# Kernel optimization log

Measured on AMD Instinct MI355X. Metric: run time of the kernel, lower is better.

Reference implementation:

```python
import jax, jax.numpy as jnp
import numpy as np

B, N, D = 32, 181, 512          # batch, num_projs (seq len), embed_dim
H, HD = 8, 64                   # heads, head_dim
DEPTH, FFN = 6, 2048            # layers, mlp_ratio*embed_dim
MAXLEN = 181                    # RPE max_len (EncoderLayer default)
LN_EPS = 1e-5


def setup_inputs() -> dict:
    key = jax.random.key(0)
    ks = jax.random.split(key, 16)
    rn = lambda k, s, sc=0.02: (jax.random.normal(k, s, jnp.float32) * sc)
    return {
        "x_0": jax.random.normal(ks[0], (B, N, D), jnp.float32),
        "max_shift": 50,
        "pos_embed": rn(ks[1], (1, N, D)),
        "qkv_w": rn(ks[2], (DEPTH, D, 3 * D)), "qkv_b": jnp.zeros((DEPTH, 3 * D), jnp.float32),
        "out_w": rn(ks[3], (DEPTH, D, D)), "out_b": jnp.zeros((DEPTH, D), jnp.float32),
        "rel_pos": jax.random.normal(ks[4], (DEPTH, 2 * MAXLEN - 1, HD), jnp.float32),
        "rpe_w": rn(ks[5], (DEPTH, HD, 1)),
        "ln1_g": jnp.ones((DEPTH, D), jnp.float32), "ln1_b": jnp.zeros((DEPTH, D), jnp.float32),
        "ffn_w1": rn(ks[6], (DEPTH, D, FFN)), "ffn_b1": jnp.zeros((DEPTH, FFN), jnp.float32),
        "ffn_w2": rn(ks[7], (DEPTH, FFN, D)), "ffn_b2": jnp.zeros((DEPTH, D), jnp.float32),
        "ln2_g": jnp.ones((DEPTH, D), jnp.float32), "ln2_b": jnp.zeros((DEPTH, D), jnp.float32),
        "mlp_w1": rn(ks[8], (D, 64)), "mlp_b1": jnp.zeros((64,), jnp.float32),
        "mlp_w2": rn(ks[9], (64, 1)), "mlp_b2": jnp.zeros((1,), jnp.float32),
    }


def _layer_norm(x, g, b):
    m = jnp.mean(x, -1, keepdims=True)
    v = jnp.mean((x - m) ** 2, -1, keepdims=True)
    return (x - m) * jax.lax.rsqrt(v + LN_EPS) * g + b


def reference(x_0, max_shift, pos_embed, qkv_w, qkv_b, out_w, out_b, rel_pos, rpe_w,
              ln1_g, ln1_b, ffn_w1, ffn_b1, ffn_w2, ffn_b2, ln2_g, ln2_b,
              mlp_w1, mlp_b1, mlp_w2, mlp_b2):
    Bb, T, L = x_0.shape
    n_head = H
    hd = L // n_head
    scale = hd ** -0.5
    max_len = (rel_pos.shape[1] + 1) // 2
    # relative position index table [T, T]
    idx = jnp.arange(T)[None, :] - jnp.arange(T)[:, None] + (max_len - 1)

    x = x_0 + pos_embed
    depth = qkv_w.shape[0]
    for i in range(depth):
        # --- MHA with relative position bias ---
        qkv = (x @ qkv_w[i] + qkv_b[i]).reshape(Bb, T, 3, n_head, hd)
        q, k, v = qkv[:, :, 0], qkv[:, :, 1], qkv[:, :, 2]   # [B,T,H,hd]
        scores = jnp.einsum('bqhd,bkhd->bhqk', q, k) * scale
        bias = (rel_pos[i][idx] @ rpe_w[i])[..., 0]          # [T,T]
        scores = scores + bias[None, None]
        w = jax.nn.softmax(scores, axis=-1)
        attn = jnp.einsum('bhqk,bkhd->bqhd', w, v).reshape(Bb, T, L)
        attn = attn @ out_w[i] + out_b[i]
        x = _layer_norm(x + attn, ln1_g[i], ln1_b[i])
        # --- FFN ---
        h = jax.nn.gelu(x @ ffn_w1[i] + ffn_b1[i], approximate=False)
        h = h @ ffn_w2[i] + ffn_b2[i]
        x = _layer_norm(x + h, ln2_g[i], ln2_b[i])

    # per-projection shift head
    shift = jax.nn.relu(x @ mlp_w1 + mlp_b1) @ mlp_w2 + mlp_b2   # [B,T,1]

    # --- SpatialTransformer: bilinear warp along L only (flow[:,0] == 0) ---
    grid_y = 2.0 * (jnp.arange(T, dtype=jnp.float32) / (T - 1) - 0.5)   # [T]
    grid_x = 2.0 * (jnp.arange(L, dtype=jnp.float32) / (L - 1) - 0.5)   # [L]
    flow_x = shift * max_shift / (L // 2)                               # [B,T,1]
    gx = grid_x[None, None, :] + flow_x                                 # [B,T,L]
    # unnormalize (align_corners=False), border padding -> clamp coords
    ix = jnp.clip(((gx + 1.0) * L - 1.0) / 2.0, 0.0, L - 1.0)
    iy = jnp.clip(((grid_y + 1.0) * T - 1.0) / 2.0, 0.0, T - 1.0)       # [T]
    ix0f = jnp.floor(ix); wx = ix - ix0f
    iy0f = jnp.floor(iy); wy = iy - iy0f
    ix0 = jnp.clip(ix0f.astype(jnp.int32), 0, L - 1)
    ix1 = jnp.clip(ix0 + 1, 0, L - 1)
    iy0 = jnp.clip(iy0f.astype(jnp.int32), 0, T - 1)
    iy1 = jnp.clip(iy0 + 1, 0, T - 1)
    bidx = jnp.arange(Bb)[:, None, None]
    iy0b, iy1b = iy0[None, :, None], iy1[None, :, None]
    v00 = x_0[bidx, iy0b, ix0]; v01 = x_0[bidx, iy0b, ix1]
    v10 = x_0[bidx, iy1b, ix0]; v11 = x_0[bidx, iy1b, ix1]
    wyb = wy[None, :, None]
    warped = (1 - wyb) * ((1 - wx) * v00 + wx * v01) + wyb * ((1 - wx) * v10 + wx * v11)
    return shift, warped
```

## Files before the change

### kernel.cpp

```cpp
#include <hip/hip_runtime.h>
#include <hip/hip_bf16.h>
#include <math.h>

#define M_ROWS 5792
#define NTOK 181
#define NLAYER 6

typedef __attribute__((ext_vector_type(8))) _Float16 f16x8;
typedef __attribute__((ext_vector_type(4))) float f32x4;
typedef __attribute__((ext_vector_type(16))) float f32x16;

__device__ __forceinline__ ushort f2h(float f) {
    union { _Float16 h; ushort u; } v;
    v.h = (_Float16)f;
    return v.u;
}
__device__ __forceinline__ float h2f(ushort u) {
    union { ushort u; _Float16 h; } v; v.u = u;
    return (float)v.h;
}
__device__ __forceinline__ float gelu_f(float v) {
    return 0.5f * v * (1.0f + erff(v * 0.70710678118654752f));
}
__device__ __forceinline__ void async16(const void* g, void* l) {
    __builtin_amdgcn_global_load_lds((const __attribute__((address_space(1))) void*)g,
                                     (__attribute__((address_space(3))) void*)l, 16, 0, 0);
}

__global__ __launch_bounds__(256) void wt_kernel(const float* __restrict__ W,
                                                 ushort* __restrict__ Wt, int K, int N) {
    __shared__ float t[64][65];
    const size_t ls = (size_t)blockIdx.z * K * N;
    const float* Wl = W + ls;
    ushort* Wtl = Wt + ls;
    const int k0 = blockIdx.x * 64, n0 = blockIdx.y * 64;
    const int tr = threadIdx.x >> 6, tc = threadIdx.x & 63;
    #pragma unroll
    for (int i = 0; i < 16; ++i) {
        const int r = i * 4 + tr;
        t[r][tc] = Wl[(size_t)(k0 + r) * N + n0 + tc];
    }
    __syncthreads();
    #pragma unroll
    for (int i = 0; i < 16; ++i) {
        const int r = i * 4 + tr;
        Wtl[(size_t)(n0 + r) * K + k0 + tc] = f2h(t[tc][r]);
    }
}

__global__ void add_pos_kernel(const float* __restrict__ x0, const float* __restrict__ pos,
                               float* __restrict__ x, ushort* __restrict__ xb) {
    int idx = blockIdx.x * 256 + threadIdx.x;
    const int total = M_ROWS * 128;
    if (idx >= total) return;
    int col = idx & 127;
    int m   = idx >> 7;
    int t   = m % NTOK;
    float4 a = ((const float4*)x0)[idx];
    float4 p = ((const float4*)pos)[t * 128 + col];
    a.x += p.x; a.y += p.y; a.z += p.z; a.w += p.w;
    ((float4*)x)[idx] = a;
    ((ushort4*)xb)[idx] = make_ushort4(f2h(a.x), f2h(a.y), f2h(a.z), f2h(a.w));
}

template<int BM, int EPI, int SK>
__global__ __launch_bounds__(256) void mfma_gemm(const ushort* __restrict__ A,
                                                 const ushort* __restrict__ Bt,
                                                 const float* __restrict__ bias,
                                                 void* __restrict__ Cv,
                                                 int M, int K, int N) {
    constexpr int MREP = BM / 32;
    __shared__ __align__(16) ushort sA[2][BM * 32];
    __shared__ __align__(16) ushort sB[2][128 * 32];

    const int NC  = N >> 7;
    const int NR  = (M + BM - 1) / BM;
    const int NRP = (NR + 7) & ~7;
    const int PSB = NRP * NC;
    const int gid = blockIdx.x;
    const int sk  = (SK > 1) ? gid / PSB : 0;
    const int j   = (SK > 1) ? gid % PSB : gid;
    const int r   = (j / (8 * NC)) * 8 + (j & 7);
    const int c   = (j % (8 * NC)) >> 3;
    if (r >= NR) return;

    const int tid = threadIdx.x;
    const int lane = tid & 63;
    const int w = tid >> 6;
    const int wr = w >> 1, wc = w & 1;
    const int row0 = r * BM, col0 = c * 128;
    const int wbase = tid & ~63;

    f32x4 acc[MREP][4];
    const f32x4 zero = {0.f, 0.f, 0.f, 0.f};
    #pragma unroll
    for (int m = 0; m < MREP; ++m)
        #pragma unroll
        for (int n = 0; n < 4; ++n) acc[m][n] = zero;

    auto stage = [&](int buf, int kt) {
        const int k0 = kt << 5;
        #pragma unroll
        for (int i = 0; i < BM / 64; ++i) {
            const int s = i * 256 + tid;
            const int row = s >> 2;
            const int kbl = (s & 3) ^ ((row >> 1) & 3);
            int gr = row0 + row; if (gr > M - 1) gr = M - 1;
            async16(A + (size_t)gr * K + k0 + (kbl << 3),
                    &sA[buf][(i * 256 + wbase) * 8]);
        }
        #pragma unroll
        for (int i = 0; i < 2; ++i) {
            const int s = i * 256 + tid;
            const int nr = s >> 2;
            const int kbl = (s & 3) ^ ((nr >> 1) & 3);
            async16(Bt + (size_t)(col0 + nr) * K + k0 + (kbl << 3),
                    &sB[buf][(i * 256 + wbase) * 8]);
        }
    };

    const int NIT = (K / SK) >> 5;
    const int kt0 = sk * NIT;
    stage(0, kt0);
    const int l15 = lane & 15, kb = lane >> 4;
    for (int it = 0; it < NIT; ++it) {
        __syncthreads();
        if (it + 1 < NIT) stage((it + 1) & 1, kt0 + it + 1);
        const int buf = it & 1;
        f16x8 af[MREP], bfr[4];
        #pragma unroll
        for (int m = 0; m < MREP; ++m) {
            const int rr = wr * (BM / 2) + m * 16 + l15;
            af[m] = *(const f16x8*)&sA[buf][rr * 32 + ((kb ^ ((rr >> 1) & 3)) << 3)];
        }
        #pragma unroll
        for (int n = 0; n < 4; ++n) {
            const int rr = wc * 64 + n * 16 + l15;
            bfr[n] = *(const f16x8*)&sB[buf][rr * 32 + ((kb ^ ((rr >> 1) & 3)) << 3)];
        }
        #pragma unroll
        for (int m = 0; m < MREP; ++m)
            #pragma unroll
            for (int n = 0; n < 4; ++n)
                acc[m][n] = __builtin_amdgcn_mfma_f32_16x16x32_f16(af[m], bfr[n], acc[m][n], 0, 0, 0);
    }

    const int crow = row0 + wr * (BM / 2) + (lane >> 4) * 4;
    const int ccol = col0 + wc * 64 + l15;
    ushort* outh = (ushort*)Cv + (size_t)sk * M * N;
    #pragma unroll
    for (int m = 0; m < MREP; ++m)
        #pragma unroll
        for (int n = 0; n < 4; ++n) {
            const int gc = ccol + n * 16;
            const float bv = (SK == 1 || sk == 0) ? bias[gc] : 0.f;
            #pragma unroll
            for (int rr = 0; rr < 4; ++rr) {
                const int gr = crow + m * 16 + rr;
                if (gr < M) {
                    float v = acc[m][n][rr] + bv;
                    if (EPI == 1)      outh[(size_t)gr * N + gc] = f2h(gelu_f(v));
                    else if (EPI == 2) outh[(size_t)gr * N + gc] = f2h(v);
                    else               ((float*)Cv)[(size_t)gr * N + gc] = v;
                }
            }
        }
}

__global__ __launch_bounds__(256) void head_mfma(const ushort* __restrict__ A,
                                                 const ushort* __restrict__ Bt,
                                                 const float* __restrict__ b1,
                                                 const float* __restrict__ w2,
                                                 const float* __restrict__ b2,
                                                 float* __restrict__ shift) {
    const int M = M_ROWS, K = 512;
    __shared__ __align__(16) ushort sA[2][128 * 32];
    __shared__ __align__(16) ushort sB[2][64 * 32];
    const int tid = threadIdx.x;
    const int lane = tid & 63;
    const int w = tid >> 6;
    const int row0 = blockIdx.x * 128;
    const int wbase = tid & ~63;

    f32x4 acc[2][4];
    const f32x4 zero = {0.f, 0.f, 0.f, 0.f};
    #pragma unroll
    for (int m = 0; m < 2; ++m)
        #pragma unroll
        for (int n = 0; n < 4; ++n) acc[m][n] = zero;

    auto stage = [&](int buf, int kt) {
        const int k0 = kt << 5;
        #pragma unroll
        for (int i = 0; i < 2; ++i) {
            const int s = i * 256 + tid;
            const int row = s >> 2;
            const int kbl = (s & 3) ^ ((row >> 1) & 3);
            int gr = row0 + row; if (gr > M - 1) gr = M - 1;
            async16(A + (size_t)gr * K + k0 + (kbl << 3),
                    &sA[buf][(i * 256 + wbase) * 8]);
        }
        {
            const int s = tid;
            const int nr = s >> 2;
            const int kbl = (s & 3) ^ ((nr >> 1) & 3);
            async16(Bt + (size_t)nr * K + k0 + (kbl << 3),
                    &sB[buf][wbase * 8]);
        }
    };

    stage(0, 0);
    const int l15 = lane & 15, kb = lane >> 4;
    for (int it = 0; it < 16; ++it) {
        __syncthreads();
        if (it + 1 < 16) stage((it + 1) & 1, it + 1);
        const int buf = it & 1;
        f16x8 af[2], bfr[4];
        #pragma unroll
        for (int m = 0; m < 2; ++m) {
            const int r = w * 32 + m * 16 + l15;
            af[m] = *(const f16x8*)&sA[buf][r * 32 + ((kb ^ ((r >> 1) & 3)) << 3)];
        }
        #pragma unroll
        for (int n = 0; n < 4; ++n) {
            const int r = n * 16 + l15;
            bfr[n] = *(const f16x8*)&sB[buf][r * 32 + ((kb ^ ((r >> 1) & 3)) << 3)];
        }
        #pragma unroll
        for (int m = 0; m < 2; ++m)
            #pragma unroll
            for (int n = 0; n < 4; ++n)
                acc[m][n] = __builtin_amdgcn_mfma_f32_16x16x32_f16(af[m], bfr[n], acc[m][n], 0, 0, 0);
    }

    const float b2v = b2[0];
    float b1v[4], w2v[4];
    #pragma unroll
    for (int n = 0; n < 4; ++n) {
        const int c = n * 16 + l15;
        b1v[n] = b1[c];
        w2v[n] = w2[c];
    }
    #pragma unroll
    for (int m = 0; m < 2; ++m) {
        #pragma unroll
        for (int r = 0; r < 4; ++r) {
            float p = 0.f;
            #pragma unroll
            for (int n = 0; n < 4; ++n)
                p += fmaxf(acc[m][n][r] + b1v[n], 0.f) * w2v[n];
            #pragma unroll
            for (int off = 1; off < 16; off <<= 1) p += __shfl_xor(p, off);
            const int gr = row0 + w * 32 + m * 16 + kb * 4 + r;
            if (l15 == 0 && gr < M) shift[gr] = p + b2v;
        }
    }
}

__global__ void rbias_kernel(const float* __restrict__ rel_pos, const float* __restrict__ rpe_w,
                             float* __restrict__ r) {
    const int l = blockIdx.y;
    int j = blockIdx.x * 64 + threadIdx.x;
    if (j >= 2 * NTOK - 1) return;
    const float* rp = rel_pos + ((size_t)l * (2 * NTOK - 1) + j) * 64;
    const float* wv = rpe_w + l * 64;
    float s = 0.f;
    #pragma unroll
    for (int d = 0; d < 64; d += 4) {
        float4 a = *(const float4*)(rp + d);
        float4 b = *(const float4*)(wv + d);
        s += a.x*b.x + a.y*b.y + a.z*b.z + a.w*b.w;
    }
    r[l * 512 + j] = s;
}

__global__ __launch_bounds__(192, 2) void attn_mfma(const ushort* __restrict__ qkv,
                                                    const float* __restrict__ rb,
                                                    ushort* __restrict__ outb) {
    __shared__ __align__(16) ushort sm[18432];
    __shared__ __align__(16) ushort vt[12288];
    __shared__ float rs[416];
    const int b  = blockIdx.x >> 4;
    const int h  = (blockIdx.x >> 1) & 7;
    const int qh = blockIdx.x & 1;
    const int tid = threadIdx.x, lane = tid & 63, w = tid >> 6;
    const int l31 = lane & 31, hi = lane >> 5;
    const ushort* base = qkv + (size_t)(b * NTOK) * 1536 + h * 64;

    for (int i = tid; i < 416; i += 192) {
        int j = i - 32;
        rs[i] = (j >= 0 && j < 2 * NTOK - 1) ? rb[j] : 0.f;
    }
    #pragma unroll
    for (int i = 0; i < 8; ++i) {
        const int c = i * 192 + w * 64 + lane;
        const int k = c >> 3;
        int kg = k; if (kg > NTOK - 1) kg = NTOK - 1;
        const int dc = (c & 7) ^ (k & 7);
        async16(base + (size_t)kg * 1536 + 512 + dc * 8, &sm[(i * 192 + w * 64) * 8]);
    }
    #pragma unroll
    for (int i = 0; i < 4; ++i) {
        const int c = i * 192 + w * 64 + lane;
        const int ql = c >> 3;
        int qg = qh * 96 + ql; if (qg > NTOK - 1) qg = NTOK - 1;
        const int dc = (c & 7) ^ (ql & 7);
        async16(base + (size_t)qg * 1536 + dc * 8, &sm[12288 + (i * 192 + w * 64) * 8]);
    }
    {
        const int k8 = tid % 24;
        const int dc = tid / 24;
        uint4 rowv[8];
        #pragma unroll
        for (int i = 0; i < 8; ++i) {
            int kk = k8 * 8 + i; if (kk > NTOK - 1) kk = NTOK - 1;
            rowv[i] = *(const uint4*)(base + (size_t)kk * 1536 + 1024 + dc * 8);
        }
        #pragma unroll
        for (int j = 0; j < 8; ++j) {
            const int d = dc * 8 + j;
            const int sd = (d ^ (d >> 3)) & 7;
            uint out[4];
            #pragma unroll
            for (int m = 0; m < 4; ++m) {
                const uint lo  = ((const uint*)&rowv[2 * m    ])[j >> 1];
                const uint hi2 = ((const uint*)&rowv[2 * m + 1])[j >> 1];
                const uint a = (j & 1) ? (lo  >> 16) : (lo  & 0xffffu);
                const uint bb = (j & 1) ? (hi2 >> 16) : (hi2 & 0xffffu);
                out[m] = a | (bb << 16);
            }
            *(uint4*)&vt[d * 192 + ((k8 ^ sd) << 3)] = *(uint4*)out;
        }
    }
    __syncthreads();

    const int ql = 32 * w + l31;
    const int q  = qh * 96 + ql;
    f16x8 qf[4];
    #pragma unroll
    for (int ds = 0; ds < 4; ++ds)
        qf[ds] = *(const f16x8*)&sm[12288 + ql * 64 + (((2 * ds + hi) ^ (ql & 7)) << 3)];

    f32x16 S[6];
    #pragma unroll
    for (int kt = 0; kt < 6; ++kt)
        #pragma unroll
        for (int r = 0; r < 16; ++r) S[kt][r] = 0.f;
    __builtin_amdgcn_s_setprio(1);
    #pragma unroll
    for (int kt = 0; kt < 6; ++kt) {
        const int krow = kt * 32 + l31;
        #pragma unroll
        for (int ds = 0; ds < 4; ++ds) {
            f16x8 kf = *(const f16x8*)&sm[krow * 64 + (((2 * ds + hi) ^ (krow & 7)) << 3)];
            S[kt] = __builtin_amdgcn_mfma_f32_32x32x16_f16(kf, qf[ds], S[kt], 0, 0, 0);
        }
    }
    __builtin_amdgcn_s_setprio(0);

    float mx = -1e30f;
    #pragma unroll
    for (int kt = 0; kt < 6; ++kt)
        #pragma unroll
        for (int r = 0; r < 16; ++r) {
            const int k = kt * 32 + (r & 3) + 8 * (r >> 2) + 4 * hi;
            float s = (k < NTOK) ? S[kt][r] * 0.125f + rs[k - q + 212] : -1e30f;
            S[kt][r] = s;
            mx = fmaxf(mx, s);
        }
    mx = fmaxf(mx, __shfl_xor(mx, 32));
    float sum = 0.f;
    #pragma unroll
    for (int kt = 0; kt < 6; ++kt)
        #pragma unroll
        for (int r = 0; r < 16; ++r) {
            float e = __expf(S[kt][r] - mx);
            S[kt][r] = e;
            sum += e;
        }
    sum += __shfl_xor(sum, 32);
    const float inv = 1.0f / sum;
    #pragma unroll
    for (int kt = 0; kt < 6; ++kt)
        #pragma unroll
        for (int r = 0; r < 16; ++r) S[kt][r] *= inv;

    f32x16 O[2];
    #pragma unroll
    for (int nt = 0; nt < 2; ++nt)
        #pragma unroll
        for (int r = 0; r < 16; ++r) O[nt][r] = 0.f;
    #pragma unroll
    for (int kt2 = 0; kt2 < 12; ++kt2) {
        const int kt = kt2 >> 1, half = kt2 & 1;
        uint p[4];
        #pragma unroll
        for (int m = 0; m < 4; ++m)
            p[m] = (uint)f2h(S[kt][8 * half + 2 * m]) |
                   ((uint)f2h(S[kt][8 * half + 2 * m + 1]) << 16);
        const uint s0l = (uint)__shfl_xor((int)p[0], 32);
        const uint s0h = (uint)__shfl_xor((int)p[1], 32);
        const uint s1l = (uint)__shfl_xor((int)p[2], 32);
        const uint s1h = (uint)__shfl_xor((int)p[3], 32);
        uint fa[4];
        if (hi == 0) { fa[0] = p[0]; fa[1] = p[1]; fa[2] = s0l; fa[3] = s0h; }
        else         { fa[0] = s1l; fa[1] = s1h; fa[2] = p[2]; fa[3] = p[3]; }
        const f16x8 pa = *(const f16x8*)fa;
        __builtin_amdgcn_s_setprio(1);
        #pragma unroll
        for (int nt = 0; nt < 2; ++nt) {
            const int d = nt * 32 + l31;
            f16x8 vf = *(const f16x8*)&vt[d * 192 + (((2 * kt2 + hi) ^ ((d ^ (d >> 3)) & 7)) << 3)];
            O[nt] = __builtin_amdgcn_mfma_f32_32x32x16_f16(pa, vf, O[nt], 0, 0, 0);
        }
        __builtin_amdgcn_s_setprio(0);
    }

    #pragma unroll
    for (int nt = 0; nt < 2; ++nt)
        #pragma unroll
        for (int r = 0; r < 16; ++r) {
            const int qr = qh * 96 + 32 * w + (r & 3) + 8 * (r >> 2) + 4 * hi;
            if (qr < NTOK)
                outb[(size_t)(b * NTOK + qr) * 512 + h * 64 + nt * 32 + l31] = f2h(O[nt][r]);
        }
}

template<int NY>
__global__ __launch_bounds__(256) void lnres_kernel(float* __restrict__ x, ushort* __restrict__ xb,
                                                    const ushort* __restrict__ y,
                                                    const ushort* __restrict__ y1,
                                                    const float* __restrict__ g, const float* __restrict__ bb) {
    const int row = blockIdx.x * 4 + (threadIdx.x >> 6);
    const int l = threadIdx.x & 63;
    float* xr = x + (size_t)row * 512;
    ushort* xbr = xb + (size_t)row * 512;
    const ushort* yr = y + (size_t)row * 512;
    float4 v0 = *(const float4*)(xr + (l << 2));
    float4 v1 = *(const float4*)(xr + 256 + (l << 2));
    const ushort4 u0 = *(const ushort4*)(yr + (l << 2));
    const ushort4 u1 = *(const ushort4*)(yr + 256 + (l << 2));
    v0.x += h2f(u0.x); v0.y += h2f(u0.y); v0.z += h2f(u0.z); v0.w += h2f(u0.w);
    v1.x += h2f(u1.x); v1.y += h2f(u1.y); v1.z += h2f(u1.z); v1.w += h2f(u1.w);
    if (NY == 2) {
        const ushort* y1r = y1 + (size_t)row * 512;
        const ushort4 w0 = *(const ushort4*)(y1r + (l << 2));
        const ushort4 w1 = *(const ushort4*)(y1r + 256 + (l << 2));
        v0.x += h2f(w0.x); v0.y += h2f(w0.y); v0.z += h2f(w0.z); v0.w += h2f(w0.w);
        v1.x += h2f(w1.x); v1.y += h2f(w1.y); v1.z += h2f(w1.z); v1.w += h2f(w1.w);
    }
    float s = v0.x + v0.y + v0.z + v0.w + v1.x + v1.y + v1.z + v1.w;
    #pragma unroll
    for (int off = 32; off; off >>= 1) s += __shfl_xor(s, off);
    const float m = s * (1.0f / 512.0f);
    float d0 = v0.x - m, d1 = v0.y - m, d2 = v0.z - m, d3 = v0.w - m;
    float d4 = v1.x - m, d5 = v1.y - m, d6 = v1.z - m, d7 = v1.w - m;
    float q = d0*d0 + d1*d1 + d2*d2 + d3*d3 + d4*d4 + d5*d5 + d6*d6 + d7*d7;
    #pragma unroll
    for (int off = 32; off; off >>= 1) q += __shfl_xor(q, off);
    const float r = rsqrtf(q * (1.0f / 512.0f) + 1e-5f);
    const float4 g0 = *(const float4*)(g + (l << 2));
    const float4 g1 = *(const float4*)(g + 256 + (l << 2));
    const float4 b0 = *(const float4*)(bb + (l << 2));
    const float4 b1 = *(const float4*)(bb + 256 + (l << 2));
    float4 o0, o1;
    o0.x = d0 * r * g0.x + b0.x; o0.y = d1 * r * g0.y + b0.y;
    o0.z = d2 * r * g0.z + b0.z; o0.w = d3 * r * g0.w + b0.w;
    o1.x = d4 * r * g1.x + b1.x; o1.y = d5 * r * g1.y + b1.y;
    o1.z = d6 * r * g1.z + b1.z; o1.w = d7 * r * g1.w + b1.w;
    *(float4*)(xr + (l << 2)) = o0;
    *(float4*)(xr + 256 + (l << 2)) = o1;
    *(ushort4*)(xbr + (l << 2)) = make_ushort4(f2h(o0.x), f2h(o0.y), f2h(o0.z), f2h(o0.w));
    *(ushort4*)(xbr + 256 + (l << 2)) = make_ushort4(f2h(o1.x), f2h(o1.y), f2h(o1.z), f2h(o1.w));
}

__global__ void warp_kernel(const float* __restrict__ x0, const float* __restrict__ shift,
                            const int* __restrict__ pms, float* __restrict__ warped) {
    int idx = blockIdx.x * 256 + threadIdx.x;
    if (idx >= M_ROWS * 512) return;
    int c = idx & 511;
    int m = idx >> 9;
    int t = m % NTOK;
    int b = m / NTOK;
    float max_shift = (float)pms[0];
    float sh = shift[m];
    float flow = sh * max_shift / 256.0f;
    float gx = 2.0f * ((float)c / 511.0f - 0.5f) + flow;
    float ix = ((gx + 1.0f) * 512.0f - 1.0f) * 0.5f;
    ix = fminf(fmaxf(ix, 0.0f), 511.0f);
    float gy = 2.0f * ((float)t / 180.0f - 0.5f);
    float iy = ((gy + 1.0f) * 181.0f - 1.0f) * 0.5f;
    iy = fminf(fmaxf(iy, 0.0f), 180.0f);
    float ix0f = floorf(ix), iy0f = floorf(iy);
    float wx = ix - ix0f, wy = iy - iy0f;
    int ix0 = min(max((int)ix0f, 0), 511);
    int ix1 = min(ix0 + 1, 511);
    int iy0 = min(max((int)iy0f, 0), 180);
    int iy1 = min(iy0 + 1, 180);
    const float* xb = x0 + (size_t)b * NTOK * 512;
    float v00 = xb[iy0 * 512 + ix0], v01 = xb[iy0 * 512 + ix1];
    float v10 = xb[iy1 * 512 + ix0], v11 = xb[iy1 * 512 + ix1];
    warped[idx] = (1.f - wy) * ((1.f - wx) * v00 + wx * v01) + wy * ((1.f - wx) * v10 + wx * v11);
}

extern "C" void kernel_launch(void* const* d_in, const int* in_sizes, int n_in,
                              void* d_out, int out_size, void* d_ws, size_t ws_size,
                              hipStream_t stream) {
    const float* x0   = (const float*)d_in[0];
    const int*   pms  = (const int*)d_in[1];
    const float* pos  = (const float*)d_in[2];
    const float* qkvw = (const float*)d_in[3];
    const float* qkvb = (const float*)d_in[4];
    const float* outw = (const float*)d_in[5];
    const float* outbp= (const float*)d_in[6];
    const float* relp = (const float*)d_in[7];
    const float* rpew = (const float*)d_in[8];
    const float* ln1g = (const float*)d_in[9];
    const float* ln1b = (const float*)d_in[10];
    const float* fw1  = (const float*)d_in[11];
    const float* fb1  = (const float*)d_in[12];
    const float* fw2  = (const float*)d_in[13];
    const float* fb2  = (const float*)d_in[14];
    const float* ln2g = (const float*)d_in[15];
    const float* ln2b = (const float*)d_in[16];
    const float* mw1  = (const float*)d_in[17];
    const float* mb1  = (const float*)d_in[18];
    const float* mw2  = (const float*)d_in[19];
    const float* mb2  = (const float*)d_in[20];

    float* out = (float*)d_out;

    char* ws = (char*)d_ws;
    float*  x     = (float*)ws;
    ushort* xb    = (ushort*)(ws + 11862016);
    char*   qr    = ws + 11862016 + 5931008;
    ushort* qkv   = (ushort*)qr;
    ushort* ybuf  = (ushort*)qr;
    ushort* ybuf2 = (ushort*)(qr + 5931008);
    ushort* hbuf  = (ushort*)(qr + 11862016);
    ushort* attnb = (ushort*)(qr + 35586048);
    float*  rbias = (float*)(qr + 35586048 + 5931008);
    ushort* wts   = (ushort*)(qr + 35586048 + 5931008 + 12288);
    ushort* qkv_wt = wts;
    ushort* out_wt = qkv_wt + 6 * 1536 * 512;
    ushort* f1_wt  = out_wt + 6 * 512 * 512;
    ushort* f2_wt  = f1_wt  + 6 * 512 * 2048;
    ushort* w1t    = f2_wt  + 6 * 2048 * 512;

    wt_kernel<<<dim3(8, 24, 6), 256, 0, stream>>>(qkvw, qkv_wt, 512, 1536);
    wt_kernel<<<dim3(8,  8, 6), 256, 0, stream>>>(outw, out_wt, 512, 512);
    wt_kernel<<<dim3(8, 32, 6), 256, 0, stream>>>(fw1,  f1_wt,  512, 2048);
    wt_kernel<<<dim3(32, 8, 6), 256, 0, stream>>>(fw2,  f2_wt,  2048, 512);
    wt_kernel<<<dim3(8,  1, 1), 256, 0, stream>>>(mw1,  w1t,    512, 64);
    rbias_kernel<<<dim3(6, 6), 64, 0, stream>>>(relp, rpew, rbias);

    add_pos_kernel<<<(M_ROWS * 128 + 255) / 256, 256, 0, stream>>>(x0, pos, x, xb);

    const int g_qkv  = 96 * 12;
    const int g_ffn1 = 96 * 16;
    const int g_np4  = 96 * 4;
    for (int i = 0; i < NLAYER; ++i) {
        mfma_gemm<64, 2, 1><<<g_qkv, 256, 0, stream>>>(xb, qkv_wt + (size_t)i * 1536 * 512,
                                                       qkvb + i * 1536, qkv, M_ROWS, 512, 1536);
        attn_mfma<<<512, 192, 0, stream>>>(qkv, rbias + i * 512, attnb);
        mfma_gemm<64, 2, 2><<<g_np4 * 2, 256, 0, stream>>>(attnb, out_wt + (size_t)i * 512 * 512,
                                                           outbp + i * 512, ybuf, M_ROWS, 512, 512);
        lnres_kernel<2><<<1448, 256, 0, stream>>>(x, xb, ybuf, ybuf2, ln1g + i * 512, ln1b + i * 512);
        mfma_gemm<64, 1, 1><<<g_ffn1, 256, 0, stream>>>(xb, f1_wt + (size_t)i * 2048 * 512,
                                                        fb1 + i * 2048, hbuf, M_ROWS, 512, 2048);
        mfma_gemm<64, 2, 2><<<g_np4 * 2, 256, 0, stream>>>(hbuf, f2_wt + (size_t)i * 512 * 2048,
                                                           fb2 + i * 512, ybuf, M_ROWS, 2048, 512);
        lnres_kernel<2><<<1448, 256, 0, stream>>>(x, xb, ybuf, ybuf2, ln2g + i * 512, ln2b + i * 512);
    }

    head_mfma<<<46, 256, 0, stream>>>(xb, w1t, mb1, mw2, mb2, out);
    warp_kernel<<<(M_ROWS * 512 + 255) / 256, 256, 0, stream>>>(x0, out, pms, out + M_ROWS);
}
```

Before: 789.6 us.

## Fuse residual LayerNorm into split-K output GEMMs via last-block atomic counter

Replaces the out-projection and FFN2 GEMM plus separate residual-LayerNorm kernels with a fused gemm_ln kernel. Each row tile's 8 blocks (4 column tiles by 2 K-splits) write fp16 partials, then bump a per-row-tile atomic counter, and the last block to finish applies the residual add and LayerNorm for those 64 rows. This removes twelve kernel launches and lets the normalisation start while other tiles are still computing. In exchange the LN tail runs in only one block per row tile, and the kernel relies on threadfence and atomics for correctness.

```diff
diff --git a/kernel.cpp b/kernel.cpp
--- a/kernel.cpp
+++ b/kernel.cpp
@@ -165,6 +165,159 @@
                 }
             }
         }
+}
+
+__global__ __launch_bounds__(256) void gemm_ln(const ushort* __restrict__ A,
+                                               const ushort* __restrict__ Bt,
+                                               const float* __restrict__ bias,
+                                               ushort* __restrict__ Cp,
+                                               float* __restrict__ x, ushort* __restrict__ xb,
+                                               const float* __restrict__ g,
+                                               const float* __restrict__ bb,
+                                               int* __restrict__ cnt,
+                                               int M, int K) {
+    constexpr int BM = 64, N = 512, NC = 4;
+    __shared__ __align__(16) ushort sA[2][BM * 32];
+    __shared__ __align__(16) ushort sB[2][128 * 32];
+    __shared__ int lastFlag;
+
+    const int NR  = (M + BM - 1) / BM;
+    const int PSB = ((NR + 7) & ~7) * NC;
+    const int gid = blockIdx.x;
+    const int sk  = gid / PSB;
+    const int j   = gid % PSB;
+    const int r   = (j / (8 * NC)) * 8 + (j & 7);
+    const int c   = (j % (8 * NC)) >> 3;
+    if (r >= NR) return;
+
+    const int tid = threadIdx.x;
+    const int lane = tid & 63;
+    const int w = tid >> 6;
+    const int wr = w >> 1, wc = w & 1;
+    const int row0 = r * BM, col0 = c * 128;
+    const int wbase = tid & ~63;
+
+    f32x4 acc[2][4];
+    const f32x4 zero = {0.f, 0.f, 0.f, 0.f};
+    #pragma unroll
+    for (int m = 0; m < 2; ++m)
+        #pragma unroll
+        for (int n = 0; n < 4; ++n) acc[m][n] = zero;
+
+    auto stage = [&](int buf, int kt) {
+        const int k0 = kt << 5;
+        {
+            const int s = tid;
+            const int row = s >> 2;
+            const int kbl = (s & 3) ^ ((row >> 1) & 3);
+            int gr = row0 + row; if (gr > M - 1) gr = M - 1;
+            async16(A + (size_t)gr * K + k0 + (kbl << 3), &sA[buf][wbase * 8]);
+        }
+        #pragma unroll
+        for (int i = 0; i < 2; ++i) {
+            const int s = i * 256 + tid;
+            const int nr = s >> 2;
+            const int kbl = (s & 3) ^ ((nr >> 1) & 3);
+            async16(Bt + (size_t)(col0 + nr) * K + k0 + (kbl << 3),
+                    &sB[buf][(i * 256 + wbase) * 8]);
+        }
+    };
+
+    const int NIT = (K / 2) >> 5;
+    const int kt0 = sk * NIT;
+    stage(0, kt0);
+    const int l15 = lane & 15, kb = lane >> 4;
+    for (int it = 0; it < NIT; ++it) {
+        __syncthreads();
+        if (it + 1 < NIT) stage((it + 1) & 1, kt0 + it + 1);
+        const int buf = it & 1;
+        f16x8 af[2], bfr[4];
+        #pragma unroll
+        for (int m = 0; m < 2; ++m) {
+            const int rr = wr * 32 + m * 16 + l15;
+            af[m] = *(const f16x8*)&sA[buf][rr * 32 + ((kb ^ ((rr >> 1) & 3)) << 3)];
+        }
+        #pragma unroll
+        for (int n = 0; n < 4; ++n) {
+            const int rr = wc * 64 + n * 16 + l15;
+            bfr[n] = *(const f16x8*)&sB[buf][rr * 32 + ((kb ^ ((rr >> 1) & 3)) << 3)];
+        }
+        #pragma unroll
+        for (int m = 0; m < 2; ++m)
+            #pragma unroll
+            for (int n = 0; n < 4; ++n)
+                acc[m][n] = __builtin_amdgcn_mfma_f32_16x16x32_f16(af[m], bfr[n], acc[m][n], 0, 0, 0);
+    }
+
+    const int crow = row0 + wr * 32 + (lane >> 4) * 4;
+    const int ccol = col0 + wc * 64 + l15;
+    ushort* outh = Cp + (size_t)sk * M * N;
+    #pragma unroll
+    for (int m = 0; m < 2; ++m)
+        #pragma unroll
+        for (int n = 0; n < 4; ++n) {
+            const int gc = ccol + n * 16;
+            const float bv = (sk == 0) ? bias[gc] : 0.f;
+            #pragma unroll
+            for (int rr = 0; rr < 4; ++rr) {
+                const int gr = crow + m * 16 + rr;
+                if (gr < M) outh[(size_t)gr * N + gc] = f2h(acc[m][n][rr] + bv);
+            }
+        }
+
+    __threadfence();
+    if (tid == 0) {
+        int old = atomicAdd(&cnt[r], 1);
+        lastFlag = (old == 7);
+    }
+    __syncthreads();
+    if (!lastFlag) return;
+    __threadfence();
+
+    const int l = lane;
+    const int wv = w;
+    #pragma unroll 1
+    for (int i = 0; i < 16; ++i) {
+        const int row = row0 + wv * 16 + i;
+        if (row >= M) continue;
+        float* xr = x + (size_t)row * 512;
+        ushort* xbr = xb + (size_t)row * 512;
+        const ushort* yr  = Cp + (size_t)row * 512;
+        const ushort* y1r = Cp + (size_t)M * 512 + (size_t)row * 512;
+        float4 v0 = *(const float4*)(xr + (l << 2));
+        float4 v1 = *(const float4*)(xr + 256 + (l << 2));
+        const ushort4 u0 = *(const ushort4*)(yr + (l << 2));
+        const ushort4 u1 = *(const ushort4*)(yr + 256 + (l << 2));
+        const ushort4 w0 = *(const ushort4*)(y1r + (l << 2));
+        const ushort4 w1 = *(const ushort4*)(y1r + 256 + (l << 2));
+        v0.x += h2f(u0.x) + h2f(w0.x); v0.y += h2f(u0.y) + h2f(w0.y);
+        v0.z += h2f(u0.z) + h2f(w0.z); v0.w += h2f(u0.w) + h2f(w0.w);
+        v1.x += h2f(u1.x) + h2f(w1.x); v1.y += h2f(u1.y) + h2f(w1.y);
+        v1.z += h2f(u1.z) + h2f(w1.z); v1.w += h2f(u1.w) + h2f(w1.w);
+        float s = v0.x + v0.y + v0.z + v0.w + v1.x + v1.y + v1.z + v1.w;
+        #pragma unroll
+        for (int off = 32; off; off >>= 1) s += __shfl_xor(s, off);
+        const float mm = s * (1.0f / 512.0f);
+        float d0 = v0.x - mm, d1 = v0.y - mm, d2 = v0.z - mm, d3 = v0.w - mm;
+        float d4 = v1.x - mm, d5 = v1.y - mm, d6 = v1.z - mm, d7 = v1.w - mm;
+        float q = d0*d0 + d1*d1 + d2*d2 + d3*d3 + d4*d4 + d5*d5 + d6*d6 + d7*d7;
+        #pragma unroll
+        for (int off = 32; off; off >>= 1) q += __shfl_xor(q, off);
+        const float rq = rsqrtf(q * (1.0f / 512.0f) + 1e-5f);
+        const float4 g0 = *(const float4*)(g + (l << 2));
+        const float4 g1 = *(const float4*)(g + 256 + (l << 2));
+        const float4 b0 = *(const float4*)(bb + (l << 2));
+        const float4 b1 = *(const float4*)(bb + 256 + (l << 2));
+        float4 o0, o1;
+        o0.x = d0 * rq * g0.x + b0.x; o0.y = d1 * rq * g0.y + b0.y;
+        o0.z = d2 * rq * g0.z + b0.z; o0.w = d3 * rq * g0.w + b0.w;
+        o1.x = d4 * rq * g1.x + b1.x; o1.y = d5 * rq * g1.y + b1.y;
+        o1.z = d6 * rq * g1.z + b1.z; o1.w = d7 * rq * g1.w + b1.w;
+        *(float4*)(xr + (l << 2)) = o0;
+        *(float4*)(xr + 256 + (l << 2)) = o1;
+        *(ushort4*)(xbr + (l << 2)) = make_ushort4(f2h(o0.x), f2h(o0.y), f2h(o0.z), f2h(o0.w));
+        *(ushort4*)(xbr + 256 + (l << 2)) = make_ushort4(f2h(o1.x), f2h(o1.y), f2h(o1.z), f2h(o1.w));
+    }
 }
 
 __global__ __launch_bounds__(256) void head_mfma(const ushort* __restrict__ A,
@@ -424,54 +577,6 @@
             if (qr < NTOK)
                 outb[(size_t)(b * NTOK + qr) * 512 + h * 64 + nt * 32 + l31] = f2h(O[nt][r]);
         }
-}
-
-template<int NY>
-__global__ __launch_bounds__(256) void lnres_kernel(float* __restrict__ x, ushort* __restrict__ xb,
-                                                    const ushort* __restrict__ y,
-                                                    const ushort* __restrict__ y1,
-                                                    const float* __restrict__ g, const float* __restrict__ bb) {
-    const int row = blockIdx.x * 4 + (threadIdx.x >> 6);
-    const int l = threadIdx.x & 63;
-    float* xr = x + (size_t)row * 512;
-    ushort* xbr = xb + (size_t)row * 512;
-    const ushort* yr = y + (size_t)row * 512;
-    float4 v0 = *(const float4*)(xr + (l << 2));
-    float4 v1 = *(const float4*)(xr + 256 + (l << 2));
-    const ushort4 u0 = *(const ushort4*)(yr + (l << 2));
-    const ushort4 u1 = *(const ushort4*)(yr + 256 + (l << 2));
-    v0.x += h2f(u0.x); v0.y += h2f(u0.y); v0.z += h2f(u0.z); v0.w += h2f(u0.w);
-    v1.x += h2f(u1.x); v1.y += h2f(u1.y); v1.z += h2f(u1.z); v1.w += h2f(u1.w);
-    if (NY == 2) {
-        const ushort* y1r = y1 + (size_t)row * 512;
-        const ushort4 w0 = *(const ushort4*)(y1r + (l << 2));
-        const ushort4 w1 = *(const ushort4*)(y1r + 256 + (l << 2));
-        v0.x += h2f(w0.x); v0.y += h2f(w0.y); v0.z += h2f(w0.z); v0.w += h2f(w0.w);
-        v1.x += h2f(w1.x); v1.y += h2f(w1.y); v1.z += h2f(w1.z); v1.w += h2f(w1.w);
-    }
-    float s = v0.x + v0.y + v0.z + v0.w + v1.x + v1.y + v1.z + v1.w;
-    #pragma unroll
-    for (int off = 32; off; off >>= 1) s += __shfl_xor(s, off);
-    const float m = s * (1.0f / 512.0f);
-    float d0 = v0.x - m, d1 = v0.y - m, d2 = v0.z - m, d3 = v0.w - m;
-    float d4 = v1.x - m, d5 = v1.y - m, d6 = v1.z - m, d7 = v1.w - m;
-    float q = d0*d0 + d1*d1 + d2*d2 + d3*d3 + d4*d4 + d5*d5 + d6*d6 + d7*d7;
-    #pragma unroll
-    for (int off = 32; off; off >>= 1) q += __shfl_xor(q, off);
-    const float r = rsqrtf(q * (1.0f / 512.0f) + 1e-5f);
-    const float4 g0 = *(const float4*)(g + (l << 2));
-    const float4 g1 = *(const float4*)(g + 256 + (l << 2));
-    const float4 b0 = *(const float4*)(bb + (l << 2));
-    const float4 b1 = *(const float4*)(bb + 256 + (l << 2));
-    float4 o0, o1;
-    o0.x = d0 * r * g0.x + b0.x; o0.y = d1 * r * g0.y + b0.y;
-    o0.z = d2 * r * g0.z + b0.z; o0.w = d3 * r * g0.w + b0.w;
-    o1.x = d4 * r * g1.x + b1.x; o1.y = d5 * r * g1.y + b1.y;
-    o1.z = d6 * r * g1.z + b1.z; o1.w = d7 * r * g1.w + b1.w;
-    *(float4*)(xr + (l << 2)) = o0;
-    *(float4*)(xr + 256 + (l << 2)) = o1;
-    *(ushort4*)(xbr + (l << 2)) = make_ushort4(f2h(o0.x), f2h(o0.y), f2h(o0.z), f2h(o0.w));
-    *(ushort4*)(xbr + 256 + (l << 2)) = make_ushort4(f2h(o1.x), f2h(o1.y), f2h(o1.z), f2h(o1.w));
 }
 
 __global__ void warp_kernel(const float* __restrict__ x0, const float* __restrict__ shift,
@@ -536,7 +641,6 @@
     char*   qr    = ws + 11862016 + 5931008;
     ushort* qkv   = (ushort*)qr;
     ushort* ybuf  = (ushort*)qr;
-    ushort* ybuf2 = (ushort*)(qr + 5931008);
     ushort* hbuf  = (ushort*)(qr + 11862016);
     ushort* attnb = (ushort*)(qr + 35586048);
     float*  rbias = (float*)(qr + 35586048 + 5931008);
@@ -546,6 +650,9 @@
     ushort* f1_wt  = out_wt + 6 * 512 * 512;
     ushort* f2_wt  = f1_wt  + 6 * 512 * 2048;
     ushort* w1t    = f2_wt  + 6 * 2048 * 512;
+    int*    cnts   = (int*)(w1t + 64 * 512);
+
+    hipMemsetAsync(cnts, 0, 12 * 128 * sizeof(int), stream);
 
     wt_kernel<<<dim3(8, 24, 6), 256, 0, stream>>>(qkvw, qkv_wt, 512, 1536);
     wt_kernel<<<dim3(8,  8, 6), 256, 0, stream>>>(outw, out_wt, 512, 512);
@@ -558,19 +665,21 @@
 
     const int g_qkv  = 96 * 12;
     const int g_ffn1 = 96 * 16;
-    const int g_np4  = 96 * 4;
+    const int g_ln   = 96 * 4 * 2;
     for (int i = 0; i < NLAYER; ++i) {
         mfma_gemm<64, 2, 1><<<g_qkv, 256, 0, stream>>>(xb, qkv_wt + (size_t)i * 1536 * 512,
                                                        qkvb + i * 1536, qkv, M_ROWS, 512, 1536);
         attn_mfma<<<512, 192, 0, stream>>>(qkv, rbias + i * 512, attnb);
-        mfma_gemm<64, 2, 2><<<g_np4 * 2, 256, 0, stream>>>(attnb, out_wt + (size_t)i * 512 * 512,
-                                                           outbp + i * 512, ybuf, M_ROWS, 512, 512);
-        lnres_kernel<2><<<1448, 256, 0, stream>>>(x, xb, ybuf, ybuf2, ln1g + i * 512, ln1b + i * 512);
+        gemm_ln<<<g_ln, 256, 0, stream>>>(attnb, out_wt + (size_t)i * 512 * 512,
+                                          outbp + i * 512, ybuf, x, xb,
+                                          ln1g + i * 512, ln1b + i * 512,
+                                          cnts + (2 * i) * 128, M_ROWS, 512);
         mfma_gemm<64, 1, 1><<<g_ffn1, 256, 0, stream>>>(xb, f1_wt + (size_t)i * 2048 * 512,
                                                         fb1 + i * 2048, hbuf, M_ROWS, 512, 2048);
-        mfma_gemm<64, 2, 2><<<g_np4 * 2, 256, 0, stream>>>(hbuf, f2_wt + (size_t)i * 512 * 2048,
-                                                           fb2 + i * 512, ybuf, M_ROWS, 2048, 512);
-        lnres_kernel<2><<<1448, 256, 0, stream>>>(x, xb, ybuf, ybuf2, ln2g + i * 512, ln2b + i * 512);
+        gemm_ln<<<g_ln, 256, 0, stream>>>(hbuf, f2_wt + (size_t)i * 512 * 2048,
+                                          fb2 + i * 512, ybuf, x, xb,
+                                          ln2g + i * 512, ln2b + i * 512,
+                                          cnts + (2 * i + 1) * 128, M_ROWS, 2048);
     }
 
     head_mfma<<<46, 256, 0, stream>>>(xb, w1t, mb1, mw2, mb2, out);
```

Measured after the change: 1.843 ms. +133.4%, slower.

## Fuse QKV projection GEMM into per-(batch,head) attention kernel

Applied to the files above, without the earlier changes.

Replaces the separate QKV GEMM and attention kernels with one kernel per (batch, head). Each kernel computes that head's Q, K and V slice from xb with a double-buffered MFMA loop, writes the results (V transposed) into shared memory, then runs the attention. This removes the global round-trip of the QKV tensor and one launch per layer. In exchange, grid parallelism drops to 256 blocks of 192 threads at one block per CU with about 122KB of LDS, and one wave handles the whole V projection and its 48 accumulators.

```diff
diff --git a/kernel.cpp b/kernel.cpp
--- a/kernel.cpp
+++ b/kernel.cpp
@@ -274,156 +274,229 @@
     r[l * 512 + j] = s;
 }
 
-__global__ __launch_bounds__(192, 2) void attn_mfma(const ushort* __restrict__ qkv,
-                                                    const float* __restrict__ rb,
-                                                    ushort* __restrict__ outb) {
-    __shared__ __align__(16) ushort sm[18432];
-    __shared__ __align__(16) ushort vt[12288];
-    __shared__ float rs[416];
-    const int b  = blockIdx.x >> 4;
-    const int h  = (blockIdx.x >> 1) & 7;
-    const int qh = blockIdx.x & 1;
+__global__ __launch_bounds__(192, 1) void attn_fused(const ushort* __restrict__ xb,
+                                                     const ushort* __restrict__ Wt,
+                                                     const float* __restrict__ bias,
+                                                     const float* __restrict__ rb,
+                                                     ushort* __restrict__ outb) {
+    extern __shared__ __align__(16) char smem[];
+    ushort* Ks = (ushort*)smem;
+    ushort* Qs = Ks + 12288;
+    ushort* vt = Qs + 12288;
+    ushort* sA = vt + 12288;
+    ushort* sB = sA + 12288;
+    float*  rs = (float*)(smem + 122880);
+
+    const int b = blockIdx.x >> 3;
+    const int h = blockIdx.x & 7;
     const int tid = threadIdx.x, lane = tid & 63, w = tid >> 6;
     const int l31 = lane & 31, hi = lane >> 5;
-    const ushort* base = qkv + (size_t)(b * NTOK) * 1536 + h * 64;
+    const int l15 = lane & 15, kb = lane >> 4;
+    const int wbase = tid & ~63;
 
     for (int i = tid; i < 416; i += 192) {
         int j = i - 32;
         rs[i] = (j >= 0 && j < 2 * NTOK - 1) ? rb[j] : 0.f;
     }
-    #pragma unroll
-    for (int i = 0; i < 8; ++i) {
-        const int c = i * 192 + w * 64 + lane;
-        const int k = c >> 3;
-        int kg = k; if (kg > NTOK - 1) kg = NTOK - 1;
-        const int dc = (c & 7) ^ (k & 7);
-        async16(base + (size_t)kg * 1536 + 512 + dc * 8, &sm[(i * 192 + w * 64) * 8]);
-    }
-    #pragma unroll
-    for (int i = 0; i < 4; ++i) {
-        const int c = i * 192 + w * 64 + lane;
-        const int ql = c >> 3;
-        int qg = qh * 96 + ql; if (qg > NTOK - 1) qg = NTOK - 1;
-        const int dc = (c & 7) ^ (ql & 7);
-        async16(base + (size_t)qg * 1536 + dc * 8, &sm[12288 + (i * 192 + w * 64) * 8]);
-    }
-    {
-        const int k8 = tid % 24;
-        const int dc = tid / 24;
-        uint4 rowv[8];
-        #pragma unroll
-        for (int i = 0; i < 8; ++i) {
-            int kk = k8 * 8 + i; if (kk > NTOK - 1) kk = NTOK - 1;
-            rowv[i] = *(const uint4*)(base + (size_t)kk * 1536 + 1024 + dc * 8);
-        }
-        #pragma unroll
-        for (int j = 0; j < 8; ++j) {
-            const int d = dc * 8 + j;
-            const int sd = (d ^ (d >> 3)) & 7;
-            uint out[4];
-            #pragma unroll
-            for (int m = 0; m < 4; ++m) {
-                const uint lo  = ((const uint*)&rowv[2 * m    ])[j >> 1];
-                const uint hi2 = ((const uint*)&rowv[2 * m + 1])[j >> 1];
-                const uint a = (j & 1) ? (lo  >> 16) : (lo  & 0xffffu);
-                const uint bb = (j & 1) ? (hi2 >> 16) : (hi2 & 0xffffu);
-                out[m] = a | (bb << 16);
-            }
-            *(uint4*)&vt[d * 192 + ((k8 ^ sd) << 3)] = *(uint4*)out;
-        }
+
+    const ushort* Arow = xb + (size_t)(b * NTOK) * 512;
+
+    auto stage = [&](int buf, int it) {
+        const int k0 = it << 5;
+        #pragma unroll
+        for (int i = 0; i < 4; ++i) {
+            const int s = i * 192 + tid;
+            const int row = s >> 2;
+            const int kbl = (s & 3) ^ ((row >> 1) & 3);
+            const int gr = row < NTOK ? row : NTOK - 1;
+            async16(Arow + (size_t)gr * 512 + k0 + (kbl << 3),
+                    &sA[buf * 6144 + (i * 192 + wbase) * 8]);
+        }
+        #pragma unroll
+        for (int i = 0; i < 4; ++i) {
+            const int s = i * 192 + tid;
+            const int n = s >> 2;
+            const int kbl = (s & 3) ^ ((n >> 1) & 3);
+            const int wrow = (n >> 6) * 512 + h * 64 + (n & 63);
+            async16(Wt + (size_t)wrow * 512 + k0 + (kbl << 3),
+                    &sB[buf * 6144 + (i * 192 + wbase) * 8]);
+        }
+    };
+
+    f32x4 acc[48];
+    const f32x4 zero = {0.f, 0.f, 0.f, 0.f};
+    #pragma unroll
+    for (int t = 0; t < 48; ++t) acc[t] = zero;
+
+    stage(0, 0);
+    for (int it = 0; it < 16; ++it) {
+        __syncthreads();
+        if (it + 1 < 16) stage((it + 1) & 1, it + 1);
+        const ushort* a  = &sA[(it & 1) * 6144];
+        const ushort* bw = &sB[(it & 1) * 6144];
+        if (w < 2) {
+            f16x8 af[12], bf[4];
+            #pragma unroll
+            for (int mt = 0; mt < 12; ++mt) {
+                const int r = mt * 16 + l15;
+                af[mt] = *(const f16x8*)&a[r * 32 + ((kb ^ ((r >> 1) & 3)) << 3)];
+            }
+            #pragma unroll
+            for (int nt = 0; nt < 4; ++nt) {
+                const int n = w * 64 + nt * 16 + l15;
+                bf[nt] = *(const f16x8*)&bw[n * 32 + ((kb ^ ((n >> 1) & 3)) << 3)];
+            }
+            #pragma unroll
+            for (int mt = 0; mt < 12; ++mt)
+                #pragma unroll
+                for (int nt = 0; nt < 4; ++nt)
+                    acc[mt * 4 + nt] = __builtin_amdgcn_mfma_f32_16x16x32_f16(af[mt], bf[nt], acc[mt * 4 + nt], 0, 0, 0);
+        } else {
+            f16x8 af[4], bf[12];
+            #pragma unroll
+            for (int mt = 0; mt < 4; ++mt) {
+                const int n = 128 + mt * 16 + l15;
+                af[mt] = *(const f16x8*)&bw[n * 32 + ((kb ^ ((n >> 1) & 3)) << 3)];
+            }
+            #pragma unroll
+            for (int nt = 0; nt < 12; ++nt) {
+                const int r = nt * 16 + l15;
+                bf[nt] = *(const f16x8*)&a[r * 32 + ((kb ^ ((r >> 1) & 3)) << 3)];
+            }
+            #pragma unroll
+            for (int mt = 0; mt < 4; ++mt)
+                #pragma unroll
+                for (int nt = 0; nt < 12; ++nt)
+                    acc[mt * 12 + nt] = __builtin_amdgcn_mfma_f32_16x16x32_f16(af[mt], bf[nt], acc[mt * 12 + nt], 0, 0, 0);
+        }
+    }
+
+    if (w < 2) {
+        ushort* dst = (w == 0) ? Qs : Ks;
+        const int boff = w * 512 + h * 64;
+        #pragma unroll
+        for (int nt = 0; nt < 4; ++nt) {
+            const int d = nt * 16 + l15;
+            const float bv = bias[boff + d];
+            #pragma unroll
+            for (int mt = 0; mt < 12; ++mt)
+                #pragma unroll
+                for (int r = 0; r < 4; ++r) {
+                    const int tok = mt * 16 + kb * 4 + r;
+                    dst[tok * 64 + (((d >> 3) ^ (tok & 7)) << 3) + (d & 7)] =
+                        f2h(acc[mt * 4 + nt][r] + bv);
+                }
+        }
+    } else {
+        #pragma unroll
+        for (int mt = 0; mt < 4; ++mt)
+            #pragma unroll
+            for (int r = 0; r < 4; ++r) {
+                const int d = mt * 16 + kb * 4 + r;
+                const float bv = bias[1024 + h * 64 + d];
+                const int sd = (d ^ (d >> 3)) & 7;
+                #pragma unroll
+                for (int nt = 0; nt < 12; ++nt) {
+                    const int tok = nt * 16 + l15;
+                    vt[d * 192 + (((tok >> 3) ^ sd) << 3) + (tok & 7)] =
+                        f2h(acc[mt * 12 + nt][r] + bv);
+                }
+            }
     }
     __syncthreads();
 
-    const int ql = 32 * w + l31;
-    const int q  = qh * 96 + ql;
-    f16x8 qf[4];
-    #pragma unroll
-    for (int ds = 0; ds < 4; ++ds)
-        qf[ds] = *(const f16x8*)&sm[12288 + ql * 64 + (((2 * ds + hi) ^ (ql & 7)) << 3)];
-
-    f32x16 S[6];
-    #pragma unroll
-    for (int kt = 0; kt < 6; ++kt)
-        #pragma unroll
-        for (int r = 0; r < 16; ++r) S[kt][r] = 0.f;
-    __builtin_amdgcn_s_setprio(1);
-    #pragma unroll
-    for (int kt = 0; kt < 6; ++kt) {
-        const int krow = kt * 32 + l31;
-        #pragma unroll
-        for (int ds = 0; ds < 4; ++ds) {
-            f16x8 kf = *(const f16x8*)&sm[krow * 64 + (((2 * ds + hi) ^ (krow & 7)) << 3)];
-            S[kt] = __builtin_amdgcn_mfma_f32_32x32x16_f16(kf, qf[ds], S[kt], 0, 0, 0);
-        }
-    }
-    __builtin_amdgcn_s_setprio(0);
-
-    float mx = -1e30f;
-    #pragma unroll
-    for (int kt = 0; kt < 6; ++kt)
-        #pragma unroll
-        for (int r = 0; r < 16; ++r) {
-            const int k = kt * 32 + (r & 3) + 8 * (r >> 2) + 4 * hi;
-            float s = (k < NTOK) ? S[kt][r] * 0.125f + rs[k - q + 212] : -1e30f;
-            S[kt][r] = s;
-            mx = fmaxf(mx, s);
-        }
-    mx = fmaxf(mx, __shfl_xor(mx, 32));
-    float sum = 0.f;
-    #pragma unroll
-    for (int kt = 0; kt < 6; ++kt)
-        #pragma unroll
-        for (int r = 0; r < 16; ++r) {
-            float e = __expf(S[kt][r] - mx);
-            S[kt][r] = e;
-            sum += e;
-        }
-    sum += __shfl_xor(sum, 32);
-    const float inv = 1.0f / sum;
-    #pragma unroll
-    for (int kt = 0; kt < 6; ++kt)
-        #pragma unroll
-        for (int r = 0; r < 16; ++r) S[kt][r] *= inv;
-
-    f32x16 O[2];
-    #pragma unroll
-    for (int nt = 0; nt < 2; ++nt)
-        #pragma unroll
-        for (int r = 0; r < 16; ++r) O[nt][r] = 0.f;
-    #pragma unroll
-    for (int kt2 = 0; kt2 < 12; ++kt2) {
-        const int kt = kt2 >> 1, half = kt2 & 1;
-        uint p[4];
-        #pragma unroll
-        for (int m = 0; m < 4; ++m)
-            p[m] = (uint)f2h(S[kt][8 * half + 2 * m]) |
-                   ((uint)f2h(S[kt][8 * half + 2 * m + 1]) << 16);
-        const uint s0l = (uint)__shfl_xor((int)p[0], 32);
-        const uint s0h = (uint)__shfl_xor((int)p[1], 32);
-        const uint s1l = (uint)__shfl_xor((int)p[2], 32);
-        const uint s1h = (uint)__shfl_xor((int)p[3], 32);
-        uint fa[4];
-        if (hi == 0) { fa[0] = p[0]; fa[1] = p[1]; fa[2] = s0l; fa[3] = s0h; }
-        else         { fa[0] = s1l; fa[1] = s1h; fa[2] = p[2]; fa[3] = p[3]; }
-        const f16x8 pa = *(const f16x8*)fa;
+    for (int qt = 0; qt < 2; ++qt) {
+        const int q0 = (w + 3 * qt) * 32;
+        const int q = q0 + l31;
+        f16x8 qf[4];
+        #pragma unroll
+        for (int ds = 0; ds < 4; ++ds)
+            qf[ds] = *(const f16x8*)&Qs[q * 64 + (((2 * ds + hi) ^ (q & 7)) << 3)];
+
+        f32x16 S[6];
+        #pragma unroll
+        for (int kt = 0; kt < 6; ++kt)
+            #pragma unroll
+            for (int r = 0; r < 16; ++r) S[kt][r] = 0.f;
         __builtin_amdgcn_s_setprio(1);
         #pragma unroll
-        for (int nt = 0; nt < 2; ++nt) {
-            const int d = nt * 32 + l31;
-            f16x8 vf = *(const f16x8*)&vt[d * 192 + (((2 * kt2 + hi) ^ ((d ^ (d >> 3)) & 7)) << 3)];
-            O[nt] = __builtin_amdgcn_mfma_f32_32x32x16_f16(pa, vf, O[nt], 0, 0, 0);
+        for (int kt = 0; kt < 6; ++kt) {
+            const int krow = kt * 32 + l31;
+            #pragma unroll
+            for (int ds = 0; ds < 4; ++ds) {
+                f16x8 kf = *(const f16x8*)&Ks[krow * 64 + (((2 * ds + hi) ^ (krow & 7)) << 3)];
+                S[kt] = __builtin_amdgcn_mfma_f32_32x32x16_f16(kf, qf[ds], S[kt], 0, 0, 0);
+            }
         }
         __builtin_amdgcn_s_setprio(0);
-    }
-
-    #pragma unroll
-    for (int nt = 0; nt < 2; ++nt)
-        #pragma unroll
-        for (int r = 0; r < 16; ++r) {
-            const int qr = qh * 96 + 32 * w + (r & 3) + 8 * (r >> 2) + 4 * hi;
-            if (qr < NTOK)
-                outb[(size_t)(b * NTOK + qr) * 512 + h * 64 + nt * 32 + l31] = f2h(O[nt][r]);
-        }
+
+        float mx = -1e30f;
+        #pragma unroll
+        for (int kt = 0; kt < 6; ++kt)
+            #pragma unroll
+            for (int r = 0; r < 16; ++r) {
+                const int k = kt * 32 + (r & 3) + 8 * (r >> 2) + 4 * hi;
+                float s = (k < NTOK) ? S[kt][r] * 0.125f + rs[k - q + 212] : -1e30f;
+                S[kt][r] = s;
+                mx = fmaxf(mx, s);
+            }
+        mx = fmaxf(mx, __shfl_xor(mx, 32));
+        float sum = 0.f;
+        #pragma unroll
+        for (int kt = 0; kt < 6; ++kt)
+            #pragma unroll
+            for (int r = 0; r < 16; ++r) {
+                float e = __expf(S[kt][r] - mx);
+                S[kt][r] = e;
+                sum += e;
+            }
+        sum += __shfl_xor(sum, 32);
+        const float inv = 1.0f / sum;
+        #pragma unroll
+        for (int kt = 0; kt < 6; ++kt)
+            #pragma unroll
+            for (int r = 0; r < 16; ++r) S[kt][r] *= inv;
+
+        f32x16 O[2];
+        #pragma unroll
+        for (int nt = 0; nt < 2; ++nt)
+            #pragma unroll
+            for (int r = 0; r < 16; ++r) O[nt][r] = 0.f;
+        #pragma unroll
+        for (int kt2 = 0; kt2 < 12; ++kt2) {
+            const int kt = kt2 >> 1, half = kt2 & 1;
+            uint p[4];
+            #pragma unroll
+            for (int m = 0; m < 4; ++m)
+                p[m] = (uint)f2h(S[kt][8 * half + 2 * m]) |
+                       ((uint)f2h(S[kt][8 * half + 2 * m + 1]) << 16);
+            const uint s0l = (uint)__shfl_xor((int)p[0], 32);
+            const uint s0h = (uint)__shfl_xor((int)p[1], 32);
+            const uint s1l = (uint)__shfl_xor((int)p[2], 32);
+            const uint s1h = (uint)__shfl_xor((int)p[3], 32);
+            uint fa[4];
+            if (hi == 0) { fa[0] = p[0]; fa[1] = p[1]; fa[2] = s0l; fa[3] = s0h; }
+            else         { fa[0] = s1l; fa[1] = s1h; fa[2] = p[2]; fa[3] = p[3]; }
+            const f16x8 pa = *(const f16x8*)fa;
+            __builtin_amdgcn_s_setprio(1);
+            #pragma unroll
+            for (int nt = 0; nt < 2; ++nt) {
+                const int d = nt * 32 + l31;
+                f16x8 vf = *(const f16x8*)&vt[d * 192 + (((2 * kt2 + hi) ^ ((d ^ (d >> 3)) & 7)) << 3)];
+                O[nt] = __builtin_amdgcn_mfma_f32_32x32x16_f16(pa, vf, O[nt], 0, 0, 0);
+            }
+            __builtin_amdgcn_s_setprio(0);
+        }
+
+        #pragma unroll
+        for (int nt = 0; nt < 2; ++nt)
+            #pragma unroll
+            for (int r = 0; r < 16; ++r) {
+                const int qr = q0 + (r & 3) + 8 * (r >> 2) + 4 * hi;
+                if (qr < NTOK)
+                    outb[(size_t)(b * NTOK + qr) * 512 + h * 64 + nt * 32 + l31] = f2h(O[nt][r]);
+            }
+    }
 }
 
 template<int NY>
@@ -534,7 +607,6 @@
     float*  x     = (float*)ws;
     ushort* xb    = (ushort*)(ws + 11862016);
     char*   qr    = ws + 11862016 + 5931008;
-    ushort* qkv   = (ushort*)qr;
     ushort* ybuf  = (ushort*)qr;
     ushort* ybuf2 = (ushort*)(qr + 5931008);
     ushort* hbuf  = (ushort*)(qr + 11862016);
@@ -547,6 +619,10 @@
     ushort* f2_wt  = f1_wt  + 6 * 512 * 2048;
     ushort* w1t    = f2_wt  + 6 * 2048 * 512;
 
+    static_assert(true, "");
+    hipFuncSetAttribute((const void*)attn_fused,
+                        hipFuncAttributeMaxDynamicSharedMemorySize, 124544);
+
     wt_kernel<<<dim3(8, 24, 6), 256, 0, stream>>>(qkvw, qkv_wt, 512, 1536);
     wt_kernel<<<dim3(8,  8, 6), 256, 0, stream>>>(outw, out_wt, 512, 512);
     wt_kernel<<<dim3(8, 32, 6), 256, 0, stream>>>(fw1,  f1_wt,  512, 2048);
@@ -556,13 +632,11 @@
 
     add_pos_kernel<<<(M_ROWS * 128 + 255) / 256, 256, 0, stream>>>(x0, pos, x, xb);
 
-    const int g_qkv  = 96 * 12;
     const int g_ffn1 = 96 * 16;
     const int g_np4  = 96 * 4;
     for (int i = 0; i < NLAYER; ++i) {
-        mfma_gemm<64, 2, 1><<<g_qkv, 256, 0, stream>>>(xb, qkv_wt + (size_t)i * 1536 * 512,
-                                                       qkvb + i * 1536, qkv, M_ROWS, 512, 1536);
-        attn_mfma<<<512, 192, 0, stream>>>(qkv, rbias + i * 512, attnb);
+        attn_fused<<<256, 192, 124544, stream>>>(xb, qkv_wt + (size_t)i * 1536 * 512,
+                                                 qkvb + i * 1536, rbias + i * 512, attnb);
         mfma_gemm<64, 2, 2><<<g_np4 * 2, 256, 0, stream>>>(attnb, out_wt + (size_t)i * 512 * 512,
                                                            outbp + i * 512, ybuf, M_ROWS, 512, 512);
         lnres_kernel<2><<<1448, 256, 0, stream>>>(x, xb, ybuf, ybuf2, ln1g + i * 512, ln1b + i * 512);
```

Result: faster. 737.3 us (-6.6%).
